# Kernel tuning notes

Hardware: AMD Instinct MI355X
Metric: run time of the kernel (lower is better)

The kernel has to match this reference:

```python
import jax, jax.numpy as jnp
import numpy as np

REMOVE_FACTOR = 1000000.0


def setup_inputs() -> dict:
    key = jax.random.key(0)
    ks = jax.random.split(key, 6)
    B, Te, Td = 4, 512, 128
    D_en, D_de, U = 256, 512, 128
    en_seq = jax.random.normal(ks[0], (B, Te, D_en), dtype=jnp.float32)
    de_seq = jax.random.normal(ks[1], (B, Td, D_de), dtype=jnp.float32)
    mask = jax.random.randint(ks[2], (B, Te), 0, 2).astype(jnp.int32)
    w_en = jax.random.normal(ks[3], (D_en, U), dtype=jnp.float32) * (1.0 / np.sqrt(D_en))
    w_de = jax.random.normal(ks[4], (D_de, U), dtype=jnp.float32) * (1.0 / np.sqrt(D_de))
    nu = jax.random.normal(ks[5], (U, 1), dtype=jnp.float32) * (1.0 / np.sqrt(U))
    return {"en_seq": en_seq, "de_seq": de_seq, "mask": mask,
            "w_en": w_en, "w_de": w_de, "nu": nu}


def reference(en_seq, de_seq, mask, w_en, w_de, nu):
    # en_seq: [B,Te,D_en], de_seq: [B,Td,D_de], mask: [B,Te] (0/1)
    m = mask.astype(en_seq.dtype)
    en = en_seq * m[..., None]                         # masked encoder states
    en_p = jnp.einsum('bte,eu->btu', en, w_en)          # [B,Te,U]
    de_p = jnp.einsum('bdf,fu->bdu', de_seq, w_de)      # [B,Td,U]
    # additive (Bahdanau) scores: scores[b,td,te] = tanh(en_p[te]+de_p[td]) @ nu
    h = jnp.tanh(en_p[:, None, :, :] + de_p[:, :, None, :])  # [B,Td,Te,U]
    mu = jnp.einsum('bdtu,u->bdt', h, nu[:, 0])               # [B,Td,Te]
    mu = mu + (m[:, None, :] - 1.0) * REMOVE_FACTOR           # mask bias
    alphas = jax.nn.softmax(mu, axis=-1)                      # softmax over Te
    sum_en = jnp.einsum('bdt,btc->bdc', alphas, en)           # [B,Td,D_en]
    return jnp.concatenate([de_seq, sum_en], axis=-1)         # [B,Td,D_de+D_en]
```

## Files before the change

### kernel.cpp

```cpp
#include <hip/hip_runtime.h>

namespace {
constexpr int B = 4, Te = 512, Td = 128, Den = 256, Dde = 512, U = 128;
constexpr float REMOVE = 1000000.0f;
constexpr float L2E2 = 2.885390081777927f;

__device__ __forceinline__ unsigned short f2bf(float f) {
  unsigned u = __float_as_uint(f);
  u += 0x7FFFu + ((u >> 16) & 1u);
  return (unsigned short)(u >> 16);
}
__device__ __forceinline__ float bf2f(unsigned short h) {
  return __uint_as_float(((unsigned)h) << 16);
}
__device__ __forceinline__ void tanh_fma(float ep, float dv, float nv, float& acc) {
  float e = __builtin_amdgcn_exp2f((ep + dv) * L2E2);
  float r = __builtin_amdgcn_rcpf(e + 1.0f);
  acc = fmaf(fmaf(-2.0f, r, 1.0f), nv, acc);
}
__device__ __forceinline__ void fma4(const float4& w, float x, float* a) {
  a[0] = fmaf(x, w.x, a[0]); a[1] = fmaf(x, w.y, a[1]);
  a[2] = fmaf(x, w.z, a[2]); a[3] = fmaf(x, w.w, a[3]);
}

__global__ __launch_bounds__(256) void proj_kernel(
    const float* __restrict__ en_seq, const float* __restrict__ de_seq,
    const int* __restrict__ mask, const float* __restrict__ w_en,
    const float* __restrict__ w_de, unsigned short* __restrict__ en_pT,
    unsigned short* __restrict__ en_bf, float* __restrict__ de_pA,
    float* __restrict__ de_pB, float* __restrict__ out) {
  __shared__ float xs[2048];
  const int blk = blockIdx.x, tid = threadIdx.x;

  if (blk < 256) {
    const int r0 = blk * 8;
    for (int i = tid; i < 512; i += 256) {
      int row = i >> 6, c4 = i & 63;
      float m = (float)mask[r0 + row];
      float4 v = *(const float4*)(en_seq + (size_t)(r0 + row) * Den + c4 * 4);
      v.x *= m; v.y *= m; v.z *= m; v.w *= m;
      *(float4*)(xs + row * 256 + c4 * 4) = v;
      ushort4 h; h.x = f2bf(v.x); h.y = f2bf(v.y); h.z = f2bf(v.z); h.w = f2bf(v.w);
      *(ushort4*)(en_bf + (size_t)(r0 + row) * Den + c4 * 4) = h;
    }
    __syncthreads();
    const int rg = tid >> 5, ug = tid & 31, u0 = ug * 4;
    float acc[4] = {0, 0, 0, 0};
#pragma unroll 4
    for (int k = 0; k < 256; k += 4) {
      const float* wp = w_en + (size_t)k * U + u0;
      float4 w0 = *(const float4*)(wp);
      float4 w1 = *(const float4*)(wp + U);
      float4 w2 = *(const float4*)(wp + 2 * U);
      float4 w3 = *(const float4*)(wp + 3 * U);
      float4 xv = *(const float4*)(xs + rg * 256 + k);
      fma4(w0, xv.x, acc); fma4(w1, xv.y, acc);
      fma4(w2, xv.z, acc); fma4(w3, xv.w, acc);
    }
    __syncthreads();
    *(float4*)(xs + rg * 128 + u0) = make_float4(acc[0], acc[1], acc[2], acc[3]);
    __syncthreads();
    {
      int u = tid >> 1, half = tid & 1;
      ushort4 h;
      h.x = f2bf(xs[(half * 4 + 0) * 128 + u]);
      h.y = f2bf(xs[(half * 4 + 1) * 128 + u]);
      h.z = f2bf(xs[(half * 4 + 2) * 128 + u]);
      h.w = f2bf(xs[(half * 4 + 3) * 128 + u]);
      int b = r0 >> 9, teT = (r0 >> 6) & 7, tein0 = r0 & 63;
      *(ushort4*)(en_pT + ((size_t)(b * 8 + teT) * 128 + u) * 64 + tein0 + half * 4) = h;
    }
  } else {
    const int q = blk - 256, rt = q >> 1, kh = q & 1;
    const int r0 = rt * 8, k0 = kh * 256;
    for (int i = tid; i < 512; i += 256) {
      int row = i >> 6, c4 = i & 63;
      float4 v = *(const float4*)(de_seq + (size_t)(r0 + row) * Dde + k0 + c4 * 4);
      *(float4*)(xs + row * 256 + c4 * 4) = v;
      *(float4*)(out + (size_t)(r0 + row) * 768 + k0 + c4 * 4) = v;
    }
    __syncthreads();
    const int rg = tid >> 5, ug = tid & 31, u0 = ug * 4;
    float acc[4] = {0, 0, 0, 0};
#pragma unroll 4
    for (int k = 0; k < 256; k += 4) {
      const float* wp = w_de + (size_t)(k0 + k) * U + u0;
      float4 w0 = *(const float4*)(wp);
      float4 w1 = *(const float4*)(wp + U);
      float4 w2 = *(const float4*)(wp + 2 * U);
      float4 w3 = *(const float4*)(wp + 3 * U);
      float4 xv = *(const float4*)(xs + rg * 256 + k);
      fma4(w0, xv.x, acc); fma4(w1, xv.y, acc);
      fma4(w2, xv.z, acc); fma4(w3, xv.w, acc);
    }
    float* dst = kh ? de_pB : de_pA;
    *(float4*)(dst + (size_t)(r0 + rg) * U + u0) =
        make_float4(acc[0], acc[1], acc[2], acc[3]);
  }
}

__global__ __launch_bounds__(256, 4) void score_kernel(
    const unsigned short* __restrict__ en_pT, const float* __restrict__ de_pA,
    const float* __restrict__ de_pB, const float* __restrict__ nu,
    const int* __restrict__ mask, float* __restrict__ mu) {
  __shared__ float tileT[128 * 64];
  __shared__ float depT[128 * 4];
  __shared__ float nus[128];
  const int blk = blockIdx.x, tid = threadIdx.x;
  const int teT = blk & 7, tdT = (blk >> 3) & 31, b = blk >> 8;
  const int te0 = teT * 64, td0 = tdT * 4;

  const unsigned short* src = en_pT + (size_t)(b * 8 + teT) * 128 * 64;
#pragma unroll
  for (int j = 0; j < 4; ++j) {
    int unit = j * 256 + tid;
    int u = unit >> 3, tc = (unit & 7) * 8;
    ushort4 ha = *(const ushort4*)(src + (size_t)u * 64 + tc);
    ushort4 hb = *(const ushort4*)(src + (size_t)u * 64 + tc + 4);
    *(float4*)(tileT + u * 64 + tc) =
        make_float4(bf2f(ha.x), bf2f(ha.y), bf2f(ha.z), bf2f(ha.w));
    *(float4*)(tileT + u * 64 + tc + 4) =
        make_float4(bf2f(hb.x), bf2f(hb.y), bf2f(hb.z), bf2f(hb.w));
  }
  for (int i = tid; i < 512; i += 256) {
    int u = i & 127, td = i >> 7;
    float v = de_pA[((size_t)b * Td + td0 + td) * U + u] +
              de_pB[((size_t)b * Td + td0 + td) * U + u];
    depT[u * 4 + td] = v;
  }
  if (tid < 128) nus[tid] = nu[tid];
  __syncthreads();

  const int tp = tid & 15, us = tid >> 4;
  const int tel0 = tp * 4;
  float a00=0,a01=0,a02=0,a03=0, a10=0,a11=0,a12=0,a13=0;
  float a20=0,a21=0,a22=0,a23=0, a30=0,a31=0,a32=0,a33=0;
#pragma unroll
  for (int jj = 0; jj < 8; ++jj) {
    int u = us + 16 * jj;
    float4 ev = *(const float4*)(tileT + u * 64 + tel0);
    float4 dv = *(const float4*)(depT + u * 4);
    float nv = nus[u];
    tanh_fma(ev.x, dv.x, nv, a00); tanh_fma(ev.y, dv.x, nv, a01);
    tanh_fma(ev.z, dv.x, nv, a02); tanh_fma(ev.w, dv.x, nv, a03);
    tanh_fma(ev.x, dv.y, nv, a10); tanh_fma(ev.y, dv.y, nv, a11);
    tanh_fma(ev.z, dv.y, nv, a12); tanh_fma(ev.w, dv.y, nv, a13);
    tanh_fma(ev.x, dv.z, nv, a20); tanh_fma(ev.y, dv.z, nv, a21);
    tanh_fma(ev.z, dv.z, nv, a22); tanh_fma(ev.w, dv.z, nv, a23);
    tanh_fma(ev.x, dv.w, nv, a30); tanh_fma(ev.y, dv.w, nv, a31);
    tanh_fma(ev.z, dv.w, nv, a32); tanh_fma(ev.w, dv.w, nv, a33);
  }
  __syncthreads();
  float* scr = tileT;
  {
    float* p = scr + us * 256 + tel0;
    p[0]   = a00; p[1]   = a01; p[2]   = a02; p[3]   = a03;
    p[64]  = a10; p[65]  = a11; p[66]  = a12; p[67]  = a13;
    p[128] = a20; p[129] = a21; p[130] = a22; p[131] = a23;
    p[192] = a30; p[193] = a31; p[194] = a32; p[195] = a33;
  }
  __syncthreads();
  {
    int td = tid >> 6, te = tid & 63;
    float s = 0.f;
#pragma unroll
    for (int q = 0; q < 16; ++q) s += scr[q * 256 + tid];
    float bias = ((float)mask[b * Te + te0 + te] - 1.0f) * REMOVE;
    mu[((size_t)b * Td + td0 + td) * Te + te0 + te] = s + bias;
  }
}

__global__ __launch_bounds__(512) void out_kernel(
    const unsigned short* __restrict__ en_bf, const int* __restrict__ mask,
    const float* __restrict__ mu, float* __restrict__ out) {
  __shared__ float al[Te * 2];
  __shared__ float scr[8 * 2 * 256];
  const int blk = blockIdx.x, tid = threadIdx.x;
  const int b = blk >> 6, tdT = blk & 63;
  const int gtd0 = b * Td + tdT * 2;
  const int wid = tid >> 6, lane = tid & 63;

  if (wid < 2) {
    const float* murow = mu + (size_t)(gtd0 + wid) * Te;
    const int* mrow = mask + b * Te;
    float v[8]; float mx = -3.0e38f;
#pragma unroll
    for (int i = 0; i < 8; ++i) { v[i] = murow[lane + i * 64]; mx = fmaxf(mx, v[i]); }
#pragma unroll
    for (int o = 32; o >= 1; o >>= 1) mx = fmaxf(mx, __shfl_xor(mx, o));
    float ss = 0.f;
#pragma unroll
    for (int i = 0; i < 8; ++i) { v[i] = __expf(v[i] - mx); ss += v[i]; }
#pragma unroll
    for (int o = 32; o >= 1; o >>= 1) ss += __shfl_xor(ss, o);
    float inv = 1.0f / ss;
#pragma unroll
    for (int i = 0; i < 8; ++i) {
      int te = lane + i * 64;
      al[te * 2 + wid] = v[i] * inv * (float)mrow[te];
    }
  }
  __syncthreads();

  {
    const int c0 = lane * 4;
    const unsigned short* eb = en_bf + (size_t)b * Te * Den + c0;
    float p0[4] = {0, 0, 0, 0}, p1[4] = {0, 0, 0, 0};
#pragma unroll 4
    for (int t = 0; t < 64; ++t) {
      int te = wid * 64 + t;
      ushort4 h = *(const ushort4*)(eb + (size_t)te * Den);
      float2 av = *(const float2*)(al + te * 2);
      float e0 = bf2f(h.x), e1 = bf2f(h.y), e2 = bf2f(h.z), e3 = bf2f(h.w);
      p0[0] = fmaf(av.x, e0, p0[0]); p0[1] = fmaf(av.x, e1, p0[1]);
      p0[2] = fmaf(av.x, e2, p0[2]); p0[3] = fmaf(av.x, e3, p0[3]);
      p1[0] = fmaf(av.y, e0, p1[0]); p1[1] = fmaf(av.y, e1, p1[1]);
      p1[2] = fmaf(av.y, e2, p1[2]); p1[3] = fmaf(av.y, e3, p1[3]);
    }
    *(float4*)(scr + (wid * 2 + 0) * 256 + c0) = make_float4(p0[0], p0[1], p0[2], p0[3]);
    *(float4*)(scr + (wid * 2 + 1) * 256 + c0) = make_float4(p1[0], p1[1], p1[2], p1[3]);
  }
  __syncthreads();

  {
    int td = tid >> 8, ch = tid & 255;
    float r = 0.f;
#pragma unroll
    for (int w = 0; w < 8; ++w) r += scr[(w * 2 + td) * 256 + ch];
    out[(size_t)(gtd0 + td) * 768 + 512 + ch] = r;
  }
}
}

extern "C" void kernel_launch(void* const* d_in, const int* in_sizes, int n_in,
                              void* d_out, int out_size, void* d_ws, size_t ws_size,
                              hipStream_t stream) {
  const float* en_seq = (const float*)d_in[0];
  const float* de_seq = (const float*)d_in[1];
  const int*   mask   = (const int*)d_in[2];
  const float* w_en   = (const float*)d_in[3];
  const float* w_de   = (const float*)d_in[4];
  const float* nu     = (const float*)d_in[5];
  float* out = (float*)d_out;

  unsigned short* en_pT = (unsigned short*)d_ws;
  unsigned short* en_bf = en_pT + (size_t)B * Te * U;
  float* de_pA = (float*)(en_bf + (size_t)B * Te * Den);
  float* de_pB = de_pA + (size_t)B * Td * U;
  float* mu    = de_pB + (size_t)B * Td * U;

  hipLaunchKernelGGL(proj_kernel, dim3(384), dim3(256), 0, stream,
                     en_seq, de_seq, mask, w_en, w_de, en_pT, en_bf,
                     de_pA, de_pB, out);
  hipLaunchKernelGGL(score_kernel, dim3(1024), dim3(256), 0, stream,
                     en_pT, de_pA, de_pB, nu, mask, mu);
  hipLaunchKernelGGL(out_kernel, dim3(256), dim3(512), 0, stream,
                     en_bf, mask, mu, out);
}
```

Baseline: 43.28 us.

## Register-block projection rows and retile output kernel across td and channel halves

The projection kernel now uses 128-thread blocks that each handle 16 rows, with every thread accumulating 4 rows. This reuses each loaded weight float4 four times and halves the number of weight reads from global memory. The output kernel now handles 4 decoder rows and half the channels per block, so each bf16 encoder element loaded is reused across 4 alpha rows. The costs are fewer blocks in the projection (192 instead of 384), which lowers parallelism, and the output kernel's softmax is repeated for each channel half.

```diff
diff --git a/kernel.cpp b/kernel.cpp
--- a/kernel.cpp
+++ b/kernel.cpp
@@ -23,18 +23,19 @@
   a[2] = fmaf(x, w.z, a[2]); a[3] = fmaf(x, w.w, a[3]);
 }
 
-__global__ __launch_bounds__(256) void proj_kernel(
+__global__ __launch_bounds__(128) void proj_kernel(
     const float* __restrict__ en_seq, const float* __restrict__ de_seq,
     const int* __restrict__ mask, const float* __restrict__ w_en,
     const float* __restrict__ w_de, unsigned short* __restrict__ en_pT,
     unsigned short* __restrict__ en_bf, float* __restrict__ de_pA,
     float* __restrict__ de_pB, float* __restrict__ out) {
-  __shared__ float xs[2048];
+  __shared__ float xs[4096];
   const int blk = blockIdx.x, tid = threadIdx.x;
-
-  if (blk < 256) {
-    const int r0 = blk * 8;
-    for (int i = tid; i < 512; i += 256) {
+  const int rg = tid >> 5, ug = tid & 31, u0 = ug * 4;
+
+  if (blk < 128) {
+    const int r0 = blk * 16;
+    for (int i = tid; i < 1024; i += 128) {
       int row = i >> 6, c4 = i & 63;
       float m = (float)mask[r0 + row];
       float4 v = *(const float4*)(en_seq + (size_t)(r0 + row) * Den + c4 * 4);
@@ -44,58 +45,70 @@
       *(ushort4*)(en_bf + (size_t)(r0 + row) * Den + c4 * 4) = h;
     }
     __syncthreads();
-    const int rg = tid >> 5, ug = tid & 31, u0 = ug * 4;
-    float acc[4] = {0, 0, 0, 0};
-#pragma unroll 4
+    float acc[4][4] = {};
     for (int k = 0; k < 256; k += 4) {
       const float* wp = w_en + (size_t)k * U + u0;
       float4 w0 = *(const float4*)(wp);
       float4 w1 = *(const float4*)(wp + U);
       float4 w2 = *(const float4*)(wp + 2 * U);
       float4 w3 = *(const float4*)(wp + 3 * U);
-      float4 xv = *(const float4*)(xs + rg * 256 + k);
-      fma4(w0, xv.x, acc); fma4(w1, xv.y, acc);
-      fma4(w2, xv.z, acc); fma4(w3, xv.w, acc);
-    }
-    __syncthreads();
-    *(float4*)(xs + rg * 128 + u0) = make_float4(acc[0], acc[1], acc[2], acc[3]);
+#pragma unroll
+      for (int j = 0; j < 4; ++j) {
+        float4 xv = *(const float4*)(xs + (rg * 4 + j) * 256 + k);
+        fma4(w0, xv.x, acc[j]); fma4(w1, xv.y, acc[j]);
+        fma4(w2, xv.z, acc[j]); fma4(w3, xv.w, acc[j]);
+      }
+    }
+    __syncthreads();
+#pragma unroll
+    for (int j = 0; j < 4; ++j)
+      *(float4*)(xs + (rg * 4 + j) * 128 + u0) =
+          make_float4(acc[j][0], acc[j][1], acc[j][2], acc[j][3]);
     __syncthreads();
     {
-      int u = tid >> 1, half = tid & 1;
-      ushort4 h;
-      h.x = f2bf(xs[(half * 4 + 0) * 128 + u]);
-      h.y = f2bf(xs[(half * 4 + 1) * 128 + u]);
-      h.z = f2bf(xs[(half * 4 + 2) * 128 + u]);
-      h.w = f2bf(xs[(half * 4 + 3) * 128 + u]);
+      int u = tid;
       int b = r0 >> 9, teT = (r0 >> 6) & 7, tein0 = r0 & 63;
-      *(ushort4*)(en_pT + ((size_t)(b * 8 + teT) * 128 + u) * 64 + tein0 + half * 4) = h;
+      unsigned short* dst =
+          en_pT + ((size_t)(b * 8 + teT) * 128 + u) * 64 + tein0;
+#pragma unroll
+      for (int q = 0; q < 4; ++q) {
+        ushort4 h;
+        h.x = f2bf(xs[(q * 4 + 0) * 128 + u]);
+        h.y = f2bf(xs[(q * 4 + 1) * 128 + u]);
+        h.z = f2bf(xs[(q * 4 + 2) * 128 + u]);
+        h.w = f2bf(xs[(q * 4 + 3) * 128 + u]);
+        *(ushort4*)(dst + q * 4) = h;
+      }
     }
   } else {
-    const int q = blk - 256, rt = q >> 1, kh = q & 1;
-    const int r0 = rt * 8, k0 = kh * 256;
-    for (int i = tid; i < 512; i += 256) {
+    const int q = blk - 128, rt = q >> 1, kh = q & 1;
+    const int r0 = rt * 16, k0 = kh * 256;
+    for (int i = tid; i < 1024; i += 128) {
       int row = i >> 6, c4 = i & 63;
       float4 v = *(const float4*)(de_seq + (size_t)(r0 + row) * Dde + k0 + c4 * 4);
       *(float4*)(xs + row * 256 + c4 * 4) = v;
       *(float4*)(out + (size_t)(r0 + row) * 768 + k0 + c4 * 4) = v;
     }
     __syncthreads();
-    const int rg = tid >> 5, ug = tid & 31, u0 = ug * 4;
-    float acc[4] = {0, 0, 0, 0};
-#pragma unroll 4
+    float acc[4][4] = {};
     for (int k = 0; k < 256; k += 4) {
       const float* wp = w_de + (size_t)(k0 + k) * U + u0;
       float4 w0 = *(const float4*)(wp);
       float4 w1 = *(const float4*)(wp + U);
       float4 w2 = *(const float4*)(wp + 2 * U);
       float4 w3 = *(const float4*)(wp + 3 * U);
-      float4 xv = *(const float4*)(xs + rg * 256 + k);
-      fma4(w0, xv.x, acc); fma4(w1, xv.y, acc);
-      fma4(w2, xv.z, acc); fma4(w3, xv.w, acc);
+#pragma unroll
+      for (int j = 0; j < 4; ++j) {
+        float4 xv = *(const float4*)(xs + (rg * 4 + j) * 256 + k);
+        fma4(w0, xv.x, acc[j]); fma4(w1, xv.y, acc[j]);
+        fma4(w2, xv.z, acc[j]); fma4(w3, xv.w, acc[j]);
+      }
     }
     float* dst = kh ? de_pB : de_pA;
-    *(float4*)(dst + (size_t)(r0 + rg) * U + u0) =
-        make_float4(acc[0], acc[1], acc[2], acc[3]);
+#pragma unroll
+    for (int j = 0; j < 4; ++j)
+      *(float4*)(dst + (size_t)(r0 + rg * 4 + j) * U + u0) =
+          make_float4(acc[j][0], acc[j][1], acc[j][2], acc[j][3]);
   }
 }
 
@@ -164,7 +177,7 @@
     int td = tid >> 6, te = tid & 63;
     float s = 0.f;
 #pragma unroll
-    for (int q = 0; q < 16; ++q) s += scr[q * 256 + tid];
+    for (int q2 = 0; q2 < 16; ++q2) s += scr[q2 * 256 + tid];
     float bias = ((float)mask[b * Te + te0 + te] - 1.0f) * REMOVE;
     mu[((size_t)b * Td + td0 + td) * Te + te0 + te] = s + bias;
   }
@@ -173,15 +186,15 @@
 __global__ __launch_bounds__(512) void out_kernel(
     const unsigned short* __restrict__ en_bf, const int* __restrict__ mask,
     const float* __restrict__ mu, float* __restrict__ out) {
-  __shared__ float al[Te * 2];
-  __shared__ float scr[8 * 2 * 256];
+  __shared__ float al[Te * 4];
+  __shared__ float part[8 * 4 * 128];
   const int blk = blockIdx.x, tid = threadIdx.x;
-  const int b = blk >> 6, tdT = blk & 63;
-  const int gtd0 = b * Td + tdT * 2;
+  const int chH = blk & 1, tdT = (blk >> 1) & 31, b = blk >> 6;
+  const int td0 = tdT * 4;
   const int wid = tid >> 6, lane = tid & 63;
 
-  if (wid < 2) {
-    const float* murow = mu + (size_t)(gtd0 + wid) * Te;
+  if (wid < 4) {
+    const float* murow = mu + (size_t)(b * Td + td0 + wid) * Te;
     const int* mrow = mask + b * Te;
     float v[8]; float mx = -3.0e38f;
 #pragma unroll
@@ -197,37 +210,39 @@
 #pragma unroll
     for (int i = 0; i < 8; ++i) {
       int te = lane + i * 64;
-      al[te * 2 + wid] = v[i] * inv * (float)mrow[te];
-    }
-  }
-  __syncthreads();
-
-  {
-    const int c0 = lane * 4;
+      al[te * 4 + wid] = v[i] * inv * (float)mrow[te];
+    }
+  }
+  __syncthreads();
+
+  {
+    const int c0 = chH * 128 + lane * 2;
     const unsigned short* eb = en_bf + (size_t)b * Te * Den + c0;
-    float p0[4] = {0, 0, 0, 0}, p1[4] = {0, 0, 0, 0};
+    float a00 = 0, a01 = 0, a10 = 0, a11 = 0, a20 = 0, a21 = 0, a30 = 0, a31 = 0;
 #pragma unroll 4
     for (int t = 0; t < 64; ++t) {
       int te = wid * 64 + t;
-      ushort4 h = *(const ushort4*)(eb + (size_t)te * Den);
-      float2 av = *(const float2*)(al + te * 2);
-      float e0 = bf2f(h.x), e1 = bf2f(h.y), e2 = bf2f(h.z), e3 = bf2f(h.w);
-      p0[0] = fmaf(av.x, e0, p0[0]); p0[1] = fmaf(av.x, e1, p0[1]);
-      p0[2] = fmaf(av.x, e2, p0[2]); p0[3] = fmaf(av.x, e3, p0[3]);
-      p1[0] = fmaf(av.y, e0, p1[0]); p1[1] = fmaf(av.y, e1, p1[1]);
-      p1[2] = fmaf(av.y, e2, p1[2]); p1[3] = fmaf(av.y, e3, p1[3]);
-    }
-    *(float4*)(scr + (wid * 2 + 0) * 256 + c0) = make_float4(p0[0], p0[1], p0[2], p0[3]);
-    *(float4*)(scr + (wid * 2 + 1) * 256 + c0) = make_float4(p1[0], p1[1], p1[2], p1[3]);
-  }
-  __syncthreads();
-
-  {
-    int td = tid >> 8, ch = tid & 255;
+      ushort2 h = *(const ushort2*)(eb + (size_t)te * Den);
+      float4 av = *(const float4*)(al + te * 4);
+      float e0 = bf2f(h.x), e1 = bf2f(h.y);
+      a00 = fmaf(av.x, e0, a00); a01 = fmaf(av.x, e1, a01);
+      a10 = fmaf(av.y, e0, a10); a11 = fmaf(av.y, e1, a11);
+      a20 = fmaf(av.z, e0, a20); a21 = fmaf(av.z, e1, a21);
+      a30 = fmaf(av.w, e0, a30); a31 = fmaf(av.w, e1, a31);
+    }
+    *(float2*)(part + (wid * 4 + 0) * 128 + lane * 2) = make_float2(a00, a01);
+    *(float2*)(part + (wid * 4 + 1) * 128 + lane * 2) = make_float2(a10, a11);
+    *(float2*)(part + (wid * 4 + 2) * 128 + lane * 2) = make_float2(a20, a21);
+    *(float2*)(part + (wid * 4 + 3) * 128 + lane * 2) = make_float2(a30, a31);
+  }
+  __syncthreads();
+
+  {
+    int td = tid >> 7, cc = tid & 127;
     float r = 0.f;
 #pragma unroll
-    for (int w = 0; w < 8; ++w) r += scr[(w * 2 + td) * 256 + ch];
-    out[(size_t)(gtd0 + td) * 768 + 512 + ch] = r;
+    for (int w = 0; w < 8; ++w) r += part[(w * 4 + td) * 128 + cc];
+    out[(size_t)(b * Td + td0 + td) * 768 + 512 + chH * 128 + cc] = r;
   }
 }
 }
@@ -249,7 +264,7 @@
   float* de_pB = de_pA + (size_t)B * Td * U;
   float* mu    = de_pB + (size_t)B * Td * U;
 
-  hipLaunchKernelGGL(proj_kernel, dim3(384), dim3(256), 0, stream,
+  hipLaunchKernelGGL(proj_kernel, dim3(192), dim3(128), 0, stream,
                      en_seq, de_seq, mask, w_en, w_de, en_pT, en_bf,
                      de_pA, de_pB, out);
   hipLaunchKernelGGL(score_kernel, dim3(1024), dim3(256), 0, stream,
```

After: 37.60 us. 1.15x faster.
